# Kernel tuning notes

Measured on AMD Instinct MI355X. Metric: run time of the kernel, lower is better.

## Reference

```python
import jax, jax.numpy as jnp
import numpy as np

NUM_USER = 50000
NUM_ITEM = 40000
N = NUM_USER + NUM_ITEM
E_HALF = 500000
DIM = 64
NUM_ROUTING = 3
NEG_SLOPE = 0.01


def setup_inputs() -> dict:
    key = jax.random.key(0)
    ks = jax.random.split(key, 10)
    rng = np.random.default_rng(0)
    u = rng.integers(0, NUM_USER, E_HALF)
    it = rng.integers(NUM_USER, N, E_HALF)
    edge_index = jnp.asarray(
        np.stack([np.concatenate([u, it]), np.concatenate([it, u])]), dtype=jnp.int64
    )  # [2, 1M] bidirected user-item edges
    return {
        "edge_index": edge_index,
        "v_feat": jax.random.normal(ks[0], (NUM_ITEM, 2048), jnp.float32),
        "t_feat": jax.random.normal(ks[1], (NUM_ITEM, 384), jnp.float32),
        "pref_v": jax.random.normal(ks[2], (NUM_USER, DIM), jnp.float32),
        "pref_t": jax.random.normal(ks[3], (NUM_USER, DIM), jnp.float32),
        "W_v": jax.random.normal(ks[4], (2048, DIM), jnp.float32) * 0.02,
        "b_v": jnp.zeros((DIM,), jnp.float32),
        "W_t": jax.random.normal(ks[5], (384, DIM), jnp.float32) * 0.05,
        "b_t": jnp.zeros((DIM,), jnp.float32),
        "id_embedding": jax.random.normal(ks[6], (N, DIM), jnp.float32),
        "conf": jax.random.normal(ks[7], (N, 2), jnp.float32),
    }


def l2norm(x, eps=1e-12):
    n = jnp.sqrt(jnp.sum(x * x, axis=1, keepdims=True))
    return x / jnp.maximum(n, eps)


def leaky_relu(x):
    return jnp.where(x >= 0, x, NEG_SLOPE * x)


def segment_softmax(logits, seg, n):
    m = jax.ops.segment_max(logits, seg, num_segments=n)
    m = jnp.where(jnp.isfinite(m), m, 0.0)  # empty segments
    e = jnp.exp(logits - jax.lax.stop_gradient(m)[seg])
    s = jax.ops.segment_sum(e, seg, num_segments=n)
    return e / (s[seg] + 1e-16)


def gat_conv(x, ei):
    # dot-product attention, segment softmax over targets, scatter-add
    src, dst = ei[0], ei[1]
    xj = x[src]  # [E, D]
    alpha = jnp.sum(x[dst] * xj, axis=-1)  # [E]
    alpha = segment_softmax(alpha, dst, x.shape[0])
    out = jax.ops.segment_sum(xj * alpha[:, None], dst, num_segments=x.shape[0])
    return out, alpha


def sage_mean(x, ei, w):
    src, dst = ei[0], ei[1]
    msg = x[src] * w  # [E, D]
    s = jax.ops.segment_sum(msg, dst, num_segments=x.shape[0])
    cnt = jax.ops.segment_sum(jnp.ones((ei.shape[1],), x.dtype), dst, num_segments=x.shape[0])
    return s / jnp.maximum(cnt, 1.0)[:, None]


def cgcn(feat, pref, W, b, ei):
    features = l2norm(leaky_relu(feat @ W + b))  # [num_item, D]
    pref = l2norm(pref)
    for _ in range(NUM_ROUTING):
        x = jnp.concatenate([pref, features], axis=0)
        xh, _ = gat_conv(x, ei)
        pref = l2norm(pref + xh[:NUM_USER])
    x = jnp.concatenate([pref, features], axis=0)
    ei2 = jnp.concatenate([ei, ei[::-1]], axis=1)  # add reversed edges
    xh, alpha = gat_conv(x, ei2)
    return x + leaky_relu(xh), alpha[:, None]


def egcn(id_emb, ei, w):
    ei2 = jnp.concatenate([ei, ei[::-1]], axis=1)
    x = l2norm(id_emb)
    h1 = leaky_relu(sage_mean(x, ei2, w))
    h2 = leaky_relu(sage_mean(h1, ei2, w))
    return x + h1 + h2


def reference(edge_index, v_feat, t_feat, pref_v, pref_t, W_v, b_v, W_t, b_t,
              id_embedding, conf):
    v_rep, weight_v = cgcn(v_feat, pref_v, W_v, b_v, edge_index)
    t_rep, weight_t = cgcn(t_feat, pref_t, W_t, b_t, edge_index)
    content_rep = jnp.concatenate([v_rep, t_rep], axis=1)  # [N, 2D]
    weight = jnp.concatenate([weight_v, weight_t], axis=1)  # [2E, 2]
    # weight_mode == 'confid'
    confidence = jnp.concatenate([conf[edge_index[0]], conf[edge_index[1]]], axis=0)
    weight = jnp.max(weight * confidence, axis=1, keepdims=True)
    weight = jax.nn.relu(weight)  # pruning
    id_rep = egcn(id_embedding, edge_index, weight)
    return jnp.concatenate([id_rep, content_rep], axis=1)  # [N, 3D]
```

## Files before the change

kernel.cpp:

```cpp
#include <hip/hip_runtime.h>
#include <hip/hip_bf16.h>
#include <cstdint>
#include <cstddef>

#define NUSER 50000
#define NITEM 40000
#define NNODE 90000
#define NE    1000000
#define DIM   64
#define CAP   32

typedef __attribute__((ext_vector_type(8))) short short8;
typedef __attribute__((ext_vector_type(4))) float f32x4;

constexpr size_t O_XVT  = 0;
constexpr size_t O_X0   = 5760000;
constexpr size_t O_X0B  = 11520000;
constexpr size_t O_H1B  = 14400000;
constexpr size_t O_XVF  = 17280000;
constexpr size_t O_XTF  = 19840000;
constexpr size_t O_AE   = 22400000;
constexpr size_t O_BE   = 23400000;
constexpr size_t O_WE   = 24400000;
constexpr size_t O_SV   = 25400000;
constexpr size_t O_ST   = 25490000;
constexpr size_t O_DEG  = 25580000;
constexpr size_t O_RP   = 25670000;
constexpr size_t O_FILL = 25770000;
constexpr size_t O_SRC  = 25870000;
constexpr size_t O_BSUM = 26870000;
constexpr size_t O_BOFF = 26871000;
constexpr size_t O_WSPL = 26880000;
constexpr size_t SW_VHI = 0;
constexpr size_t SW_VLO = 131072;
constexpr size_t SW_THI = 262144;
constexpr size_t SW_TLO = 286720;

__device__ __forceinline__ float leaky(float x) { return x >= 0.f ? x : 0.01f * x; }

__device__ __forceinline__ unsigned short f2bfu(float x) {
  __hip_bfloat16 h = __float2bfloat16(x);
  return *reinterpret_cast<unsigned short*>(&h);
}
__device__ __forceinline__ short f2bf(float x) { return (short)f2bfu(x); }
__device__ __forceinline__ float bf2f(short s) {
  unsigned int u = ((unsigned int)(unsigned short)s) << 16;
  return __uint_as_float(u);
}
__device__ __forceinline__ void bf8_to_f32(uint4 u, float* f) {
  f[0] = __uint_as_float(u.x << 16); f[1] = __uint_as_float(u.x & 0xffff0000u);
  f[2] = __uint_as_float(u.y << 16); f[3] = __uint_as_float(u.y & 0xffff0000u);
// ... 7 lines not shown
  u.z = (uint32_t)f2bfu(f[4]) | ((uint32_t)f2bfu(f[5]) << 16);
  u.w = (uint32_t)f2bfu(f[6]) | ((uint32_t)f2bfu(f[7]) << 16);
  return u;
}
__device__ __forceinline__ void bf4_to_f32(uint2 u, float* f) {
  f[0] = __uint_as_float(u.x << 16); f[1] = __uint_as_float(u.x & 0xffff0000u);
  f[2] = __uint_as_float(u.y << 16); f[3] = __uint_as_float(u.y & 0xffff0000u);
}
__device__ __forceinline__ uint2 f32_to_bf4(const float* f) {
  uint2 u;
  u.x = (uint32_t)f2bfu(f[0]) | ((uint32_t)f2bfu(f[1]) << 16);
  u.y = (uint32_t)f2bfu(f[2]) | ((uint32_t)f2bfu(f[3]) << 16);
  return u;
}

__global__ void deg_count_kernel(const int* __restrict__ ei, int* __restrict__ deg) {
  int e = blockIdx.x * 256 + threadIdx.x;
  if (e >= NE) return;
  atomicAdd(&deg[ei[NE + e]], 1);
}

__global__ void block_sum_kernel(const int* __restrict__ deg, int* __restrict__ bsum) {
  __shared__ int sd[4];
  int i = blockIdx.x * 256 + threadIdx.x;
  int v = (i < NNODE) ? deg[i] : 0;
#pragma unroll
  for (int off = 32; off > 0; off >>= 1) v += __shfl_xor(v, off, 64);
  if ((threadIdx.x & 63) == 0) sd[threadIdx.x >> 6] = v;
  __syncthreads();
  if (threadIdx.x == 0) bsum[blockIdx.x] = sd[0] + sd[1] + sd[2] + sd[3];
}

__global__ void scan_bsum_kernel(const int* __restrict__ bsum, int* __restrict__ boff, int nb) {
  __shared__ int s[512];
  int t = threadIdx.x;
  int v = (t < nb) ? bsum[t] : 0;
  s[t] = v;
  __syncthreads();
  for (int off = 1; off < 512; off <<= 1) {
    int x = (t >= off) ? s[t - off] : 0;
    __syncthreads();
    s[t] += x;
    __syncthreads();
  }
  if (t < nb) boff[t] = s[t] - v;
}

__global__ void scan_final_kernel(const int* __restrict__ deg, const int* __restrict__ boff,
                                  int* __restrict__ row_ptr, int* __restrict__ fill) {
  __shared__ int s[256];
  int t = threadIdx.x;
  int i = blockIdx.x * 256 + t;
  int v = (i < NNODE) ? deg[i] : 0;
  s[t] = v;
  __syncthreads();
  for (int off = 1; off < 256; off <<= 1) {
    int x = (t >= off) ? s[t - off] : 0;
    __syncthreads();
    s[t] += x;
    __syncthreads();
  }
  int incl = s[t];
  int base = boff[blockIdx.x];
  if (i < NNODE) {
    row_ptr[i] = base + incl - v;
    fill[i] = base + incl - v;
    if (i == NNODE - 1) row_ptr[NNODE] = base + incl;
  }
}

__global__ void csr_fill_kernel(const int* __restrict__ ei, int* __restrict__ fill,
                                int* __restrict__ srcs) {
  int e = blockIdx.x * 256 + threadIdx.x;
  if (e >= NE) return;
  int s = ei[e], d = ei[NE + e];
  int slot = atomicAdd(&fill[d], 1);
  srcs[slot] = s;
}

__global__ void wsplit_kernel(const float* __restrict__ W, short* __restrict__ hi,
                              short* __restrict__ lo, int nelem) {
  int t = blockIdx.x * 256 + threadIdx.x;
  if (t >= nelem) return;
  int j = t & 7, sl = (t >> 3) & 15, q = (t >> 7) & 3, nt = (t >> 9) & 3, kt = t >> 11;
  int k = kt * 32 + q * 8 + j, n = nt * 16 + sl;
  float x = W[k * 64 + n];
  short h = f2bf(x);
  hi[t] = h;
  lo[t] = f2bf(x - bf2f(h));
}

__global__ __launch_bounds__(256) void gemm_mfma_kernel(const float* __restrict__ A,
                                                        const short* __restrict__ Whi,
                                                        const short* __restrict__ Wlo,
                                                        const float* __restrict__ bias,
                                                        float* __restrict__ outF,
                                                        unsigned short* __restrict__ xvt,
                                                        int colbase, int K) {
  __shared__ short Bsh[8192];
  __shared__ short Bsl[8192];
  int tid = threadIdx.x;
  int w = tid >> 6, lane = tid & 63, q = lane >> 4, sl = lane & 15;
  int m0 = blockIdx.x * 64;
  const float* arow = A + (size_t)(m0 + w * 16 + sl) * K;
  f32x4 acc[4] = {{0.f, 0.f, 0.f, 0.f}, {0.f, 0.f, 0.f, 0.f},
                  {0.f, 0.f, 0.f, 0.f}, {0.f, 0.f, 0.f, 0.f}};
  int nchunk = K >> 7;
  for (int c = 0; c < nchunk; ++c) {
    __syncthreads();
    const float4* srch = (const float4*)(Whi + (size_t)c * 8192);
    const float4* srcl = (const float4*)(Wlo + (size_t)c * 8192);
    float4* dsth = (float4*)Bsh;
    float4* dstl = (float4*)Bsl;
#pragma unroll
    for (int r = 0; r < 4; ++r) {
      dsth[r * 256 + tid] = srch[r * 256 + tid];
      dstl[r * 256 + tid] = srcl[r * 256 + tid];
    }
    __syncthreads();
#pragma unroll
    for (int kt = 0; kt < 4; ++kt) {
      int k = c * 128 + kt * 32 + q * 8;
// ... 5 lines not shown
      for (int j = 0; j < 8; ++j) {
        short h = f2bf(av[j]);
        ah[j] = h;
        al[j] = f2bf(av[j] - bf2f(h));
      }
#pragma unroll
      for (int nt = 0; nt < 4; ++nt) {
        short8 bh = *(short8*)&Bsh[(kt * 4 + nt) * 512 + lane * 8];
        short8 bl = *(short8*)&Bsl[(kt * 4 + nt) * 512 + lane * 8];
        acc[nt] = __builtin_amdgcn_mfma_f32_16x16x32_bf16(ah, bh, acc[nt], 0, 0, 0);
        acc[nt] = __builtin_amdgcn_mfma_f32_16x16x32_bf16(ah, bl, acc[nt], 0, 0, 0);
        acc[nt] = __builtin_amdgcn_mfma_f32_16x16x32_bf16(al, bh, acc[nt], 0, 0, 0);
      }
    }
  }
  float bnt[4];
#pragma unroll
  for (int nt = 0; nt < 4; ++nt) bnt[nt] = bias[nt * 16 + sl];
  float v[4][4];
#pragma unroll
  for (int nt = 0; nt < 4; ++nt)
#pragma unroll
    for (int i = 0; i < 4; ++i) v[nt][i] = leaky(acc[nt][i] + bnt[nt]);
#pragma unroll
  for (int i = 0; i < 4; ++i) {
    float ss = v[0][i] * v[0][i] + v[1][i] * v[1][i] + v[2][i] * v[2][i] + v[3][i] * v[3][i];
    ss += __shfl_xor(ss, 1);
    ss += __shfl_xor(ss, 2);
    ss += __shfl_xor(ss, 4);
    ss += __shfl_xor(ss, 8);
    float rinv = 1.f / fmaxf(sqrtf(ss), 1e-12f);
    int row = m0 + w * 16 + q * 4 + i;
#pragma unroll
    for (int nt = 0; nt < 4; ++nt) {
      float val = v[nt][i] * rinv;
      outF[(size_t)row * 64 + nt * 16 + sl] = val;
      xvt[(size_t)(NUSER + row) * 128 + colbase + nt * 16 + sl] = f2bfu(val);
    }
  }
}

__global__ __launch_bounds__(256) void l2norm_id_kernel(const float* __restrict__ id,
                                                        float* __restrict__ x0,
                                                        unsigned short* __restrict__ X0b) {
  int wid = (blockIdx.x * 256 + threadIdx.x) >> 6;
  int lane = threadIdx.x & 63, sub = lane >> 4, sl = lane & 15;
  int r = wid * 4 + sub;
  if (r >= NNODE) return;
  float4 v = *(const float4*)&id[(size_t)r * 64 + sl * 4];
  float ss = v.x * v.x + v.y * v.y + v.z * v.z + v.w * v.w;
  ss += __shfl_xor(ss, 1);
  ss += __shfl_xor(ss, 2);
  ss += __shfl_xor(ss, 4);
  ss += __shfl_xor(ss, 8);
  float rinv = 1.f / fmaxf(sqrtf(ss), 1e-12f);
  float f[4] = {v.x * rinv, v.y * rinv, v.z * rinv, v.w * rinv};
  *(float4*)&x0[(size_t)r * 64 + sl * 4] = *(float4*)f;
  *(uint2*)&X0b[(size_t)r * 64 + sl * 4] = f32_to_bf4(f);
}

__global__ __launch_bounds__(256) void routing_user_kernel(
    const float* __restrict__ pref_v, const float* __restrict__ pref_t,
    unsigned short* __restrict__ XVT,
    const int* __restrict__ rp, const int* __restrict__ srcs,
    const float* __restrict__ conf,
    float* __restrict__ Ae, float* __restrict__ Be,
    float* __restrict__ SV, float* __restrict__ ST,
    float* __restrict__ out) {
  __shared__ unsigned short cache[4][CAP * 128];
  int wv = threadIdx.x >> 6;
  int u = blockIdx.x * 4 + wv;
  if (u >= NUSER) return;
  int lane = threadIdx.x & 63;
  int sub = lane >> 4, sl = lane & 15, half = sl >> 3, e8 = sl & 7;
  unsigned short* myc = cache[wv];

  const float* psrc = half ? pref_t : pref_v;
  float p[8];
  *(float4*)&p[0] = *(const float4*)&psrc[(size_t)u * 64 + e8 * 8];
  *(float4*)&p[4] = *(const float4*)&psrc[(size_t)u * 64 + e8 * 8 + 4];
  float ss = 0.f;
#pragma unroll
  for (int k = 0; k < 8; ++k) ss += p[k] * p[k];
  ss += __shfl_xor(ss, 1); ss += __shfl_xor(ss, 2); ss += __shfl_xor(ss, 4);
  float rinv = 1.f / fmaxf(sqrtf(ss), 1e-12f);
#pragma unroll
  for (int k = 0; k < 8; ++k) p[k] *= rinv;

  int jb = rp[u], je = rp[u + 1], deg = je - jb;

  for (int it = 0; it < 3; ++it) {
    float S = 0.f;
    float acc[8] = {0.f, 0.f, 0.f, 0.f, 0.f, 0.f, 0.f, 0.f};
    for (int i0 = 0; i0 < deg; i0 += 4) {
      int i = i0 + sub;
      bool valid = i < deg;
      int ii = valid ? i : 0;
      int j = jb + ii;
      int s = srcs[j];
      uint4 u4;
      if (it == 0) {
        u4 = *(const uint4*)&XVT[(size_t)s * 128 + sl * 8];
        if (valid && i < CAP) *(uint4*)&myc[i * 128 + sl * 8] = u4;
      } else {
        if (ii < CAP) u4 = *(const uint4*)&myc[ii * 128 + sl * 8];
        else u4 = *(const uint4*)&XVT[(size_t)s * 128 + sl * 8];
      }
      float f[8];
      bf8_to_f32(u4, f);
      float d = 0.f;
#pragma unroll
      for (int k = 0; k < 8; ++k) d += p[k] * f[k];
      d += __shfl_xor(d, 1); d += __shfl_xor(d, 2); d += __shfl_xor(d, 4);
      float e = valid ? __expf(d) : 0.f;
      S += e;
#pragma unroll
      for (int k = 0; k < 8; ++k) acc[k] += e * f[k];
    }
    S += __shfl_xor(S, 16); S += __shfl_xor(S, 32);
#pragma unroll
    for (int k = 0; k < 8; ++k) {
      acc[k] += __shfl_xor(acc[k], 16);
      acc[k] += __shfl_xor(acc[k], 32);
    }
    if (deg > 0) {
      float r = 1.f / S;
#pragma unroll
      for (int k = 0; k < 8; ++k) p[k] += acc[k] * r;
    }
    ss = 0.f;
#pragma unroll
    for (int k = 0; k < 8; ++k) ss += p[k] * p[k];
    ss += __shfl_xor(ss, 1); ss += __shfl_xor(ss, 2); ss += __shfl_xor(ss, 4);
    rinv = 1.f / fmaxf(sqrtf(ss), 1e-12f);
#pragma unroll
    for (int k = 0; k < 8; ++k) p[k] *= rinv;
  }

  float S = 0.f;
  float acc[8] = {0.f, 0.f, 0.f, 0.f, 0.f, 0.f, 0.f, 0.f};
  for (int i0 = 0; i0 < deg; i0 += 4) {
    int i = i0 + sub;
    bool valid = i < deg;
    int ii = valid ? i : 0;
    int j = jb + ii;
    int s = srcs[j];
    uint4 u4;
    if (ii < CAP) u4 = *(const uint4*)&myc[ii * 128 + sl * 8];
    else u4 = *(const uint4*)&XVT[(size_t)s * 128 + sl * 8];
    float f[8];
    bf8_to_f32(u4, f);
    float d = 0.f;
#pragma unroll
    for (int k = 0; k < 8; ++k) d += p[k] * f[k];
    d += __shfl_xor(d, 1); d += __shfl_xor(d, 2); d += __shfl_xor(d, 4);
    float dot_o = __shfl_xor(d, 8);
    float e = valid ? __expf(d) : 0.f;
    S += e;
#pragma unroll
    for (int k = 0; k < 8; ++k) acc[k] += e * f[k];
    if (valid && sl == 0) {
      float2 c = *(const float2*)&conf[2 * s];
      Ae[j] = e * c.x;
      Be[j] = __expf(dot_o) * c.y;
    }
  }
  S += __shfl_xor(S, 16); S += __shfl_xor(S, 32);
#pragma unroll
  for (int k = 0; k < 8; ++k) {
    acc[k] += __shfl_xor(acc[k], 16);
    acc[k] += __shfl_xor(acc[k], 32);
  }
  float St = __shfl(S, 8);
  if (lane == 0) { SV[u] = S; ST[u] = St; }
  if (sub == 0) {
    float o[8];
    if (deg > 0) {
      float r = 1.f / S;
#pragma unroll
      for (int k = 0; k < 8; ++k) o[k] = p[k] + leaky(acc[k] * r);
    } else {
#pragma unroll
      for (int k = 0; k < 8; ++k) o[k] = p[k];
    }
    size_t ob = (size_t)u * 192 + 64 + half * 64 + e8 * 8;
    *(float4*)&out[ob] = *(float4*)&o[0];
    *(float4*)&out[ob + 4] = *(float4*)&o[4];
    *(uint4*)&XVT[(size_t)u * 128 + sl * 8] = f32_to_bf8(p);
  }
}

__global__ __launch_bounds__(256) void gat_item_kernel(
    const unsigned short* __restrict__ XVT,
    const float* __restrict__ XVf, const float* __restrict__ XTf,
    const int* __restrict__ rp, const int* __restrict__ srcs,
    const float* __restrict__ conf,
    float* __restrict__ Ae, float* __restrict__ Be,
    float* __restrict__ SV, float* __restrict__ ST,
    float* __restrict__ out) {
  int wid = (blockIdx.x * 256 + threadIdx.x) >> 6;
  if (wid >= NITEM) return;
  int lane = threadIdx.x & 63;
  int sub = lane >> 4, sl = lane & 15, half = sl >> 3, e8 = sl & 7;
  int row = NUSER + wid;
  const float* xsrc = half ? XTf : XVf;
  float xn[8];
  *(float4*)&xn[0] = *(const float4*)&xsrc[(size_t)wid * 64 + e8 * 8];
  *(float4*)&xn[4] = *(const float4*)&xsrc[(size_t)wid * 64 + e8 * 8 + 4];
  int jb = rp[row], je = rp[row + 1], deg = je - jb;
  float S = 0.f;
  float acc[8] = {0.f, 0.f, 0.f, 0.f, 0.f, 0.f, 0.f, 0.f};
  for (int i0 = 0; i0 < deg; i0 += 4) {
    int i = i0 + sub;
    bool valid = i < deg;
    int j = jb + (valid ? i : 0);
    int s = srcs[j];
    uint4 u4 = *(const uint4*)&XVT[(size_t)s * 128 + sl * 8];
    float f[8];
    bf8_to_f32(u4, f);
    float d = 0.f;
#pragma unroll
    for (int k = 0; k < 8; ++k) d += xn[k] * f[k];
    d += __shfl_xor(d, 1); d += __shfl_xor(d, 2); d += __shfl_xor(d, 4);
    float dot_o = __shfl_xor(d, 8);
    float e = valid ? __expf(d) : 0.f;
    S += e;
#pragma unroll
    for (int k = 0; k < 8; ++k) acc[k] += e * f[k];
    if (valid && sl == 0) {
      float2 c = *(const float2*)&conf[2 * s];
      Ae[j] = e * c.x;
      Be[j] = __expf(dot_o) * c.y;
    }
  }
  S += __shfl_xor(S, 16); S += __shfl_xor(S, 32);
#pragma unroll
  for (int k = 0; k < 8; ++k) {
    acc[k] += __shfl_xor(acc[k], 16);
    acc[k] += __shfl_xor(acc[k], 32);
  }
  float St = __shfl(S, 8);
  if (lane == 0) { SV[row] = S; ST[row] = St; }
  if (sub == 0) {
    float o[8];
    if (deg > 0) {
      float r = 1.f / S;
#pragma unroll
      for (int k = 0; k < 8; ++k) o[k] = xn[k] + leaky(acc[k] * r);
    } else {
#pragma unroll
      for (int k = 0; k < 8; ++k) o[k] = xn[k];
    }
    size_t ob = (size_t)row * 192 + 64 + half * 64 + e8 * 8;
    *(float4*)&out[ob] = *(float4*)&o[0];
    *(float4*)&out[ob + 4] = *(float4*)&o[4];
  }
}

__global__ __launch_bounds__(256) void egcn_h1_kernel(
    const unsigned short* __restrict__ X0b,
    const int* __restrict__ rp, const int* __restrict__ srcs,
    const float* __restrict__ Ae, const float* __restrict__ Be,
    const float* __restrict__ SV, const float* __restrict__ ST,
    float* __restrict__ wE, unsigned short* __restrict__ H1b) {
  int wid = (blockIdx.x * 256 + threadIdx.x) >> 6;
  if (wid >= NNODE) return;
  int lane = threadIdx.x & 63, sub = lane >> 4, sl = lane & 15;
  int jb = rp[wid], je = rp[wid + 1], deg = je - jb;
  float rv = 0.f, rt = 0.f;
  if (deg > 0) { rv = 0.5f / SV[wid]; rt = 0.5f / ST[wid]; }
  float acc[4] = {0.f, 0.f, 0.f, 0.f};
  for (int i0 = 0; i0 < deg; i0 += 4) {
    int i = i0 + sub;
    bool valid = i < deg;
    int j = jb + (valid ? i : 0);
    int s = srcs[j];
    float w = fmaxf(fmaxf(rv * Ae[j], rt * Be[j]), 0.f);
    if (!valid) w = 0.f;
    if (valid && sl == 0) wE[j] = w;
    uint2 u2 = *(const uint2*)&X0b[(size_t)s * 64 + sl * 4];
    float f[4];
    bf4_to_f32(u2, f);
#pragma unroll
    for (int k = 0; k < 4; ++k) acc[k] += w * f[k];
  }
#pragma unroll
  for (int k = 0; k < 4; ++k) {
    acc[k] += __shfl_xor(acc[k], 16);
    acc[k] += __shfl_xor(acc[k], 32);
  }
  if (sub == 0) {
    float h[4] = {0.f, 0.f, 0.f, 0.f};
    if (deg > 0) {
      float r = 1.f / (float)deg;
#pragma unroll
      for (int k = 0; k < 4; ++k) h[k] = leaky(acc[k] * r);
    }
    *(uint2*)&H1b[(size_t)wid * 64 + sl * 4] = f32_to_bf4(h);
  }
}

__global__ __launch_bounds__(256) void egcn_h2_kernel(
    const float* __restrict__ x0, const unsigned short* __restrict__ H1b,
    const int* __restrict__ rp, const int* __restrict__ srcs,
    const float* __restrict__ wE, float* __restrict__ out) {
  int wid = (blockIdx.x * 256 + threadIdx.x) >> 6;
  if (wid >= NNODE) return;
  int lane = threadIdx.x & 63, sub = lane >> 4, sl = lane & 15;
  int jb = rp[wid], je = rp[wid + 1], deg = je - jb;
  float acc[4] = {0.f, 0.f, 0.f, 0.f};
  for (int i0 = 0; i0 < deg; i0 += 4) {
    int i = i0 + sub;
    bool valid = i < deg;
    int j = jb + (valid ? i : 0);
    int s = srcs[j];
    float w = valid ? wE[j] : 0.f;
    uint2 u2 = *(const uint2*)&H1b[(size_t)s * 64 + sl * 4];
    float f[4];
    bf4_to_f32(u2, f);
#pragma unroll
    for (int k = 0; k < 4; ++k) acc[k] += w * f[k];
  }
#pragma unroll
  for (int k = 0; k < 4; ++k) {
    acc[k] += __shfl_xor(acc[k], 16);
    acc[k] += __shfl_xor(acc[k], 32);
  }
  if (sub == 0) {
    float h2[4] = {0.f, 0.f, 0.f, 0.f};
    if (deg > 0) {
      float r = 1.f / (float)deg;
#pragma unroll
      for (int k = 0; k < 4; ++k) h2[k] = leaky(acc[k] * r);
    }
    float4 a = *(const float4*)&x0[(size_t)wid * 64 + sl * 4];
    uint2 u2 = *(const uint2*)&H1b[(size_t)wid * 64 + sl * 4];
// ... 26 lines not shown
  float* x0 = ws + O_X0;
  unsigned short* X0b = (unsigned short*)(ws + O_X0B);
  unsigned short* H1b = (unsigned short*)(ws + O_H1B);
  float* XVf = ws + O_XVF;
  float* XTf = ws + O_XTF;
  float* Ae = ws + O_AE;
  float* Be = ws + O_BE;
  float* wE = ws + O_WE;
  float* SV = ws + O_SV;
  float* ST = ws + O_ST;
  int* deg = (int*)(ws + O_DEG);
  int* row_ptr = (int*)(ws + O_RP);
  int* fill = (int*)(ws + O_FILL);
  int* srcs = (int*)(ws + O_SRC);
  int* bsum = (int*)(ws + O_BSUM);
  int* boff = (int*)(ws + O_BOFF);
  short* wsp = (short*)(ws + O_WSPL);
  short* WvHi = wsp + SW_VHI;
  short* WvLo = wsp + SW_VLO;
  short* WtHi = wsp + SW_THI;
  short* WtLo = wsp + SW_TLO;

  const int NB = (NNODE + 255) / 256;

  hipMemsetAsync(deg, 0, NNODE * sizeof(int), stream);
  deg_count_kernel<<<(NE + 255) / 256, 256, 0, stream>>>(ei, deg);
  block_sum_kernel<<<NB, 256, 0, stream>>>(deg, bsum);
  scan_bsum_kernel<<<1, 512, 0, stream>>>(bsum, boff, NB);
  scan_final_kernel<<<NB, 256, 0, stream>>>(deg, boff, row_ptr, fill);
  csr_fill_kernel<<<(NE + 255) / 256, 256, 0, stream>>>(ei, fill, srcs);

  wsplit_kernel<<<(2048 * 64 + 255) / 256, 256, 0, stream>>>(W_v, WvHi, WvLo, 2048 * 64);
  wsplit_kernel<<<(384 * 64 + 255) / 256, 256, 0, stream>>>(W_t, WtHi, WtLo, 384 * 64);

  gemm_mfma_kernel<<<NITEM / 64, 256, 0, stream>>>(v_feat, WvHi, WvLo, b_v, XVf, XVT, 0, 2048);
  gemm_mfma_kernel<<<NITEM / 64, 256, 0, stream>>>(t_feat, WtHi, WtLo, b_t, XTf, XVT, 64, 384);

  l2norm_id_kernel<<<NNODE / 16, 256, 0, stream>>>(id_emb, x0, X0b);

  routing_user_kernel<<<NUSER / 4, 256, 0, stream>>>(pref_v, pref_t, XVT, row_ptr, srcs, conf,
                                                     Ae, Be, SV, ST, out);

  gat_item_kernel<<<NITEM / 4, 256, 0, stream>>>(XVT, XVf, XTf, row_ptr, srcs, conf,
                                                 Ae, Be, SV, ST, out);

  egcn_h1_kernel<<<NNODE / 4, 256, 0, stream>>>(X0b, row_ptr, srcs, Ae, Be, SV, ST, wE, H1b);
  egcn_h2_kernel<<<NNODE / 4, 256, 0, stream>>>(x0, H1b, row_ptr, srcs, wE, out);
}
```

Measured before the change: 973.0 us.

## Fuse preprocessing into mega kernel, split-K GEMM, fold EGCN h1 into GAT kernels

Several changes land together. Degree counting, l2norm of the id embeddings and both feature GEMMs now run as branches of one multi-role kernel, and the v_feat GEMM is split along K into four partial sums. The bias, leaky ReLU and l2norm epilogue moves into a separate kernel that also fills the CSR, and the scan is cut to two kernels. The EGCN h1 aggregation is folded into the user and item attention kernels, reading edge weights from a per-wave shared-memory stash, and the gather loops are unrolled by two. This removes launches and the separate h1 pass and spreads the GEMM over more blocks, at the cost of an extra partial-sum buffer round trip through memory.

Result: faster. 893.6 us (-8.2%).

```diff
diff --git a/kernel.cpp b/kernel.cpp
--- a/kernel.cpp
+++ b/kernel.cpp
@@ -9,6 +9,7 @@
 #define NE    1000000
 #define DIM   64
 #define CAP   32
+#define ESTN  128
 
 typedef __attribute__((ext_vector_type(8))) short short8;
 typedef __attribute__((ext_vector_type(4))) float f32x4;
@@ -29,12 +30,22 @@
 constexpr size_t O_FILL = 25770000;
 constexpr size_t O_SRC  = 25870000;
 constexpr size_t O_BSUM = 26870000;
-constexpr size_t O_BOFF = 26871000;
 constexpr size_t O_WSPL = 26880000;
+constexpr size_t O_PV   = 27040000;
+constexpr size_t O_PT   = 37280000;
 constexpr size_t SW_VHI = 0;
 constexpr size_t SW_VLO = 131072;
 constexpr size_t SW_THI = 262144;
 constexpr size_t SW_TLO = 286720;
+
+#define B_GV 2500
+#define B_GT 625
+#define B_DC 1024
+#define B_LN 1024
+#define BASE_GT 2500
+#define BASE_DC 3125
+#define BASE_LN 4149
+#define MEGA_BLOCKS 5173
 
 __device__ __forceinline__ float leaky(float x) { return x >= 0.f ? x : 0.01f * x; }
 
@@ -72,98 +83,36 @@
   return u;
 }
 
-__global__ void deg_count_kernel(const int* __restrict__ ei, int* __restrict__ deg) {
-  int e = blockIdx.x * 256 + threadIdx.x;
-  if (e >= NE) return;
-  atomicAdd(&deg[ei[NE + e]], 1);
-}
-
-__global__ void block_sum_kernel(const int* __restrict__ deg, int* __restrict__ bsum) {
-  __shared__ int sd[4];
-  int i = blockIdx.x * 256 + threadIdx.x;
-  int v = (i < NNODE) ? deg[i] : 0;
-#pragma unroll
-  for (int off = 32; off > 0; off >>= 1) v += __shfl_xor(v, off, 64);
-  if ((threadIdx.x & 63) == 0) sd[threadIdx.x >> 6] = v;
-  __syncthreads();
-  if (threadIdx.x == 0) bsum[blockIdx.x] = sd[0] + sd[1] + sd[2] + sd[3];
-}
-
-__global__ void scan_bsum_kernel(const int* __restrict__ bsum, int* __restrict__ boff, int nb) {
-  __shared__ int s[512];
-  int t = threadIdx.x;
-  int v = (t < nb) ? bsum[t] : 0;
-  s[t] = v;
-  __syncthreads();
-  for (int off = 1; off < 512; off <<= 1) {
-    int x = (t >= off) ? s[t - off] : 0;
-    __syncthreads();
-    s[t] += x;
-    __syncthreads();
-  }
-  if (t < nb) boff[t] = s[t] - v;
-}
-
-__global__ void scan_final_kernel(const int* __restrict__ deg, const int* __restrict__ boff,
-                                  int* __restrict__ row_ptr, int* __restrict__ fill) {
-  __shared__ int s[256];
-  int t = threadIdx.x;
-  int i = blockIdx.x * 256 + t;
-  int v = (i < NNODE) ? deg[i] : 0;
-  s[t] = v;
-  __syncthreads();
-  for (int off = 1; off < 256; off <<= 1) {
-    int x = (t >= off) ? s[t - off] : 0;
-    __syncthreads();
-    s[t] += x;
-    __syncthreads();
-  }
-  int incl = s[t];
-  int base = boff[blockIdx.x];
-  if (i < NNODE) {
-    row_ptr[i] = base + incl - v;
-    fill[i] = base + incl - v;
-    if (i == NNODE - 1) row_ptr[NNODE] = base + incl;
-  }
-}
-
-__global__ void csr_fill_kernel(const int* __restrict__ ei, int* __restrict__ fill,
-                                int* __restrict__ srcs) {
-  int e = blockIdx.x * 256 + threadIdx.x;
-  if (e >= NE) return;
-  int s = ei[e], d = ei[NE + e];
-  int slot = atomicAdd(&fill[d], 1);
-  srcs[slot] = s;
-}
-
-__global__ void wsplit_kernel(const float* __restrict__ W, short* __restrict__ hi,
-                              short* __restrict__ lo, int nelem) {
+__global__ __launch_bounds__(256) void wsplit_all_kernel(const float* __restrict__ Wv,
+                                                         const float* __restrict__ Wt,
+                                                         short* __restrict__ base) {
   int t = blockIdx.x * 256 + threadIdx.x;
-  if (t >= nelem) return;
-  int j = t & 7, sl = (t >> 3) & 15, q = (t >> 7) & 3, nt = (t >> 9) & 3, kt = t >> 11;
+  const int NV = 2048 * 64, NT = 384 * 64;
+  const float* W;
+  short *hi, *lo;
+  int idx;
+  if (t < NV) { W = Wv; hi = base + SW_VHI; lo = base + SW_VLO; idx = t; }
+  else if (t < NV + NT) { W = Wt; hi = base + SW_THI; lo = base + SW_TLO; idx = t - NV; }
+  else return;
+  int j = idx & 7, sl = (idx >> 3) & 15, q = (idx >> 7) & 3, nt = (idx >> 9) & 3, kt = idx >> 11;
   int k = kt * 32 + q * 8 + j, n = nt * 16 + sl;
   float x = W[k * 64 + n];
   short h = f2bf(x);
-  hi[t] = h;
-  lo[t] = f2bf(x - bf2f(h));
-}
-
-__global__ __launch_bounds__(256) void gemm_mfma_kernel(const float* __restrict__ A,
-                                                        const short* __restrict__ Whi,
-                                                        const short* __restrict__ Wlo,
-                                                        const float* __restrict__ bias,
-                                                        float* __restrict__ outF,
-                                                        unsigned short* __restrict__ xvt,
-                                                        int colbase, int K) {
-  __shared__ short Bsh[8192];
-  __shared__ short Bsl[8192];
+  hi[idx] = h;
+  lo[idx] = f2bf(x - bf2f(h));
+}
+
+__device__ __forceinline__ void gemm_partial(const float* __restrict__ A,
+                                             const short* __restrict__ Whi,
+                                             const short* __restrict__ Wlo,
+                                             float* __restrict__ P, size_t prow0,
+                                             short* Bsh, short* Bsl,
+                                             int m0, int K, int kofs, int nchunk) {
   int tid = threadIdx.x;
   int w = tid >> 6, lane = tid & 63, q = lane >> 4, sl = lane & 15;
-  int m0 = blockIdx.x * 64;
-  const float* arow = A + (size_t)(m0 + w * 16 + sl) * K;
+  const float* arow = A + (size_t)(m0 + w * 16 + sl) * K + kofs;
   f32x4 acc[4] = {{0.f, 0.f, 0.f, 0.f}, {0.f, 0.f, 0.f, 0.f},
                   {0.f, 0.f, 0.f, 0.f}, {0.f, 0.f, 0.f, 0.f}};
-  int nchunk = K >> 7;
   for (int c = 0; c < nchunk; ++c) {
     __syncthreads();
     const float4* srch = (const float4*)(Whi + (size_t)c * 8192);
@@ -199,66 +148,158 @@
       }
     }
   }
-  float bnt[4];
-#pragma unroll
-  for (int nt = 0; nt < 4; ++nt) bnt[nt] = bias[nt * 16 + sl];
-  float v[4][4];
-#pragma unroll
-  for (int nt = 0; nt < 4; ++nt)
-#pragma unroll
-    for (int i = 0; i < 4; ++i) v[nt][i] = leaky(acc[nt][i] + bnt[nt]);
 #pragma unroll
   for (int i = 0; i < 4; ++i) {
-    float ss = v[0][i] * v[0][i] + v[1][i] * v[1][i] + v[2][i] * v[2][i] + v[3][i] * v[3][i];
-    ss += __shfl_xor(ss, 1);
-    ss += __shfl_xor(ss, 2);
-    ss += __shfl_xor(ss, 4);
-    ss += __shfl_xor(ss, 8);
-    float rinv = 1.f / fmaxf(sqrtf(ss), 1e-12f);
     int row = m0 + w * 16 + q * 4 + i;
 #pragma unroll
-    for (int nt = 0; nt < 4; ++nt) {
-      float val = v[nt][i] * rinv;
-      outF[(size_t)row * 64 + nt * 16 + sl] = val;
-      xvt[(size_t)(NUSER + row) * 128 + colbase + nt * 16 + sl] = f2bfu(val);
-    }
-  }
-}
-
-__global__ __launch_bounds__(256) void l2norm_id_kernel(const float* __restrict__ id,
-                                                        float* __restrict__ x0,
-                                                        unsigned short* __restrict__ X0b) {
-  int wid = (blockIdx.x * 256 + threadIdx.x) >> 6;
-  int lane = threadIdx.x & 63, sub = lane >> 4, sl = lane & 15;
-  int r = wid * 4 + sub;
-  if (r >= NNODE) return;
-  float4 v = *(const float4*)&id[(size_t)r * 64 + sl * 4];
-  float ss = v.x * v.x + v.y * v.y + v.z * v.z + v.w * v.w;
-  ss += __shfl_xor(ss, 1);
-  ss += __shfl_xor(ss, 2);
-  ss += __shfl_xor(ss, 4);
-  ss += __shfl_xor(ss, 8);
+    for (int nt = 0; nt < 4; ++nt)
+      P[(prow0 + row) * 64 + nt * 16 + sl] = acc[nt][i];
+  }
+}
+
+__global__ __launch_bounds__(256) void mega_prep_kernel(
+    const float* __restrict__ v_feat, const float* __restrict__ t_feat,
+    const short* __restrict__ wsp,
+    const int* __restrict__ ei, int* __restrict__ deg,
+    const float* __restrict__ id_emb, float* __restrict__ x0,
+    unsigned short* __restrict__ X0b,
+    float* __restrict__ Pv, float* __restrict__ Pt) {
+  __shared__ short Bsh[8192];
+  __shared__ short Bsl[8192];
+  int b = blockIdx.x;
+  if (b < B_GV) {
+    int seg = b / 625, m0 = (b % 625) * 64;
+    gemm_partial(v_feat, wsp + SW_VHI + (size_t)seg * 4 * 8192,
+                 wsp + SW_VLO + (size_t)seg * 4 * 8192,
+                 Pv, (size_t)seg * 40000, Bsh, Bsl, m0, 2048, seg * 512, 4);
+  } else if (b < BASE_DC) {
+    int m0 = (b - BASE_GT) * 64;
+    gemm_partial(t_feat, wsp + SW_THI, wsp + SW_TLO, Pt, 0, Bsh, Bsl, m0, 384, 0, 3);
+  } else if (b < BASE_LN) {
+    for (int e = (b - BASE_DC) * 256 + threadIdx.x; e < NE; e += B_DC * 256)
+      atomicAdd(&deg[ei[NE + e]], 1);
+  } else {
+    int sl = threadIdx.x & 15;
+    int qg = (b - BASE_LN) * 16 + (threadIdx.x >> 4);
+    for (int r = qg; r < NNODE; r += B_LN * 16) {
+      float4 v = *(const float4*)&id_emb[(size_t)r * 64 + sl * 4];
+      float ss = v.x * v.x + v.y * v.y + v.z * v.z + v.w * v.w;
+      ss += __shfl_xor(ss, 1); ss += __shfl_xor(ss, 2);
+      ss += __shfl_xor(ss, 4); ss += __shfl_xor(ss, 8);
+      float rinv = 1.f / fmaxf(sqrtf(ss), 1e-12f);
+      float f[4] = {v.x * rinv, v.y * rinv, v.z * rinv, v.w * rinv};
+      *(float4*)&x0[(size_t)r * 64 + sl * 4] = *(float4*)f;
+      *(uint2*)&X0b[(size_t)r * 64 + sl * 4] = f32_to_bf4(f);
+    }
+  }
+}
+
+__global__ __launch_bounds__(256) void scan_a_kernel(const int* __restrict__ deg,
+                                                     int* __restrict__ bsum) {
+  __shared__ int sd[4];
+  int i = blockIdx.x * 256 + threadIdx.x;
+  int v = (i < NNODE) ? deg[i] : 0;
+#pragma unroll
+  for (int off = 32; off > 0; off >>= 1) v += __shfl_xor(v, off, 64);
+  if ((threadIdx.x & 63) == 0) sd[threadIdx.x >> 6] = v;
+  __syncthreads();
+  if (threadIdx.x == 0) bsum[blockIdx.x] = sd[0] + sd[1] + sd[2] + sd[3];
+}
+
+__global__ __launch_bounds__(256) void scan_b_kernel(const int* __restrict__ deg,
+                                                     const int* __restrict__ bsum,
+                                                     int* __restrict__ row_ptr,
+                                                     int* __restrict__ fill) {
+  __shared__ int s[256];
+  __shared__ int sbase[4];
+  int t = threadIdx.x, b = blockIdx.x;
+  int v = (t < b) ? bsum[t] : 0;
+  if (t + 256 < b) v += bsum[t + 256];
+#pragma unroll
+  for (int off = 32; off > 0; off >>= 1) v += __shfl_xor(v, off, 64);
+  if ((t & 63) == 0) sbase[t >> 6] = v;
+  int i = b * 256 + t;
+  int d = (i < NNODE) ? deg[i] : 0;
+  s[t] = d;
+  __syncthreads();
+  int base = sbase[0] + sbase[1] + sbase[2] + sbase[3];
+  for (int off = 1; off < 256; off <<= 1) {
+    int x = (t >= off) ? s[t - off] : 0;
+    __syncthreads();
+    s[t] += x;
+    __syncthreads();
+  }
+  if (i < NNODE) {
+    int excl = base + s[t] - d;
+    row_ptr[i] = excl;
+    fill[i] = excl;
+    if (i == NNODE - 1) row_ptr[NNODE] = base + s[t];
+  }
+}
+
+#define FE_FILL 512
+__global__ __launch_bounds__(256) void fill_epi_kernel(
+    const int* __restrict__ ei, int* __restrict__ fill, int* __restrict__ srcs,
+    const float* __restrict__ Pv, const float* __restrict__ Pt,
+    const float* __restrict__ b_v, const float* __restrict__ b_t,
+    float* __restrict__ XVf, float* __restrict__ XTf,
+    unsigned short* __restrict__ XVT) {
+  int b = blockIdx.x;
+  if (b < FE_FILL) {
+    for (int e = b * 256 + threadIdx.x; e < NE; e += FE_FILL * 256) {
+      int s = ei[e], d = ei[NE + e];
+      int slot = atomicAdd(&fill[d], 1);
+      srcs[slot] = s;
+    }
+    return;
+  }
+  int sl = threadIdx.x & 15;
+  int q = (b - FE_FILL) * 16 + (threadIdx.x >> 4);
+  if (q >= 80000) return;
+  int mod = q >= 40000;
+  int r = q - mod * 40000;
+  float4 a;
+  if (!mod) {
+    a = *(const float4*)&Pv[(size_t)r * 64 + sl * 4];
+#pragma unroll
+    for (int seg = 1; seg < 4; ++seg) {
+      float4 p = *(const float4*)&Pv[((size_t)seg * 40000 + r) * 64 + sl * 4];
+      a.x += p.x; a.y += p.y; a.z += p.z; a.w += p.w;
+    }
+  } else {
+    a = *(const float4*)&Pt[(size_t)r * 64 + sl * 4];
+  }
+  float4 bias = *(const float4*)&(mod ? b_t : b_v)[sl * 4];
+  float f[4] = {leaky(a.x + bias.x), leaky(a.y + bias.y),
+                leaky(a.z + bias.z), leaky(a.w + bias.w)};
+  float ss = f[0] * f[0] + f[1] * f[1] + f[2] * f[2] + f[3] * f[3];
+  ss += __shfl_xor(ss, 1); ss += __shfl_xor(ss, 2);
+  ss += __shfl_xor(ss, 4); ss += __shfl_xor(ss, 8);
   float rinv = 1.f / fmaxf(sqrtf(ss), 1e-12f);
-  float f[4] = {v.x * rinv, v.y * rinv, v.z * rinv, v.w * rinv};
-  *(float4*)&x0[(size_t)r * 64 + sl * 4] = *(float4*)f;
-  *(uint2*)&X0b[(size_t)r * 64 + sl * 4] = f32_to_bf4(f);
+#pragma unroll
+  for (int k = 0; k < 4; ++k) f[k] *= rinv;
+  *(float4*)&(mod ? XTf : XVf)[(size_t)r * 64 + sl * 4] = *(float4*)f;
+  *(uint2*)&XVT[(size_t)(NUSER + r) * 128 + mod * 64 + sl * 4] = f32_to_bf4(f);
 }
 
 __global__ __launch_bounds__(256) void routing_user_kernel(
     const float* __restrict__ pref_v, const float* __restrict__ pref_t,
-    unsigned short* __restrict__ XVT,
+    unsigned short* __restrict__ XVT, const unsigned short* __restrict__ X0b,
     const int* __restrict__ rp, const int* __restrict__ srcs,
     const float* __restrict__ conf,
     float* __restrict__ Ae, float* __restrict__ Be,
     float* __restrict__ SV, float* __restrict__ ST,
+    float* __restrict__ wE, unsigned short* __restrict__ H1b,
     float* __restrict__ out) {
   __shared__ unsigned short cache[4][CAP * 128];
+  __shared__ float estash[4][2 * ESTN];
   int wv = threadIdx.x >> 6;
   int u = blockIdx.x * 4 + wv;
   if (u >= NUSER) return;
   int lane = threadIdx.x & 63;
   int sub = lane >> 4, sl = lane & 15, half = sl >> 3, e8 = sl & 7;
   unsigned short* myc = cache[wv];
+  float* es = estash[wv];
 
   const float* psrc = half ? pref_t : pref_v;
   float p[8];
@@ -277,30 +318,37 @@
   for (int it = 0; it < 3; ++it) {
     float S = 0.f;
     float acc[8] = {0.f, 0.f, 0.f, 0.f, 0.f, 0.f, 0.f, 0.f};
-    for (int i0 = 0; i0 < deg; i0 += 4) {
-      int i = i0 + sub;
-      bool valid = i < deg;
-      int ii = valid ? i : 0;
-      int j = jb + ii;
-      int s = srcs[j];
-      uint4 u4;
+    for (int i0 = 0; i0 < deg; i0 += 8) {
+      int iA = i0 + sub, iB = i0 + 4 + sub;
+      bool vA = iA < deg, vB = iB < deg;
+      int jA = jb + (vA ? iA : 0), jB = jb + (vB ? iB : 0);
+      uint4 uA, uB;
       if (it == 0) {
-        u4 = *(const uint4*)&XVT[(size_t)s * 128 + sl * 8];
-        if (valid && i < CAP) *(uint4*)&myc[i * 128 + sl * 8] = u4;
+        int sA = srcs[jA], sB = srcs[jB];
+        uA = *(const uint4*)&XVT[(size_t)sA * 128 + sl * 8];
+        uB = *(const uint4*)&XVT[(size_t)sB * 128 + sl * 8];
+        if (vA && iA < CAP) *(uint4*)&myc[iA * 128 + sl * 8] = uA;
+        if (vB && iB < CAP) *(uint4*)&myc[iB * 128 + sl * 8] = uB;
       } else {
-        if (ii < CAP) u4 = *(const uint4*)&myc[ii * 128 + sl * 8];
-        else u4 = *(const uint4*)&XVT[(size_t)s * 128 + sl * 8];
+        int iiA = vA ? iA : 0, iiB = vB ? iB : 0;
+        if (iiA < CAP) uA = *(const uint4*)&myc[iiA * 128 + sl * 8];
+        else uA = *(const uint4*)&XVT[(size_t)srcs[jA] * 128 + sl * 8];
+        if (iiB < CAP) uB = *(const uint4*)&myc[iiB * 128 + sl * 8];
+        else uB = *(const uint4*)&XVT[(size_t)srcs[jB] * 128 + sl * 8];
       }
-      float f[8];
-      bf8_to_f32(u4, f);
-      float d = 0.f;
-#pragma unroll
-      for (int k = 0; k < 8; ++k) d += p[k] * f[k];
-      d += __shfl_xor(d, 1); d += __shfl_xor(d, 2); d += __shfl_xor(d, 4);
-      float e = valid ? __expf(d) : 0.f;
-      S += e;
-#pragma unroll
-      for (int k = 0; k < 8; ++k) acc[k] += e * f[k];
+      float fA[8], fB[8];
+      bf8_to_f32(uA, fA);
+      bf8_to_f32(uB, fB);
+      float dA = 0.f, dB = 0.f;
+#pragma unroll
+      for (int k = 0; k < 8; ++k) { dA += p[k] * fA[k]; dB += p[k] * fB[k]; }
+      dA += __shfl_xor(dA, 1); dA += __shfl_xor(dA, 2); dA += __shfl_xor(dA, 4);
+      dB += __shfl_xor(dB, 1); dB += __shfl_xor(dB, 2); dB += __shfl_xor(dB, 4);
+      float eA = vA ? __expf(dA) : 0.f;
+      float eB = vB ? __expf(dB) : 0.f;
+      S += eA + eB;
+#pragma unroll
+      for (int k = 0; k < 8; ++k) acc[k] += eA * fA[k] + eB * fB[k];
     }
     S += __shfl_xor(S, 16); S += __shfl_xor(S, 32);
 #pragma unroll
@@ -324,30 +372,44 @@
 
   float S = 0.f;
   float acc[8] = {0.f, 0.f, 0.f, 0.f, 0.f, 0.f, 0.f, 0.f};
-  for (int i0 = 0; i0 < deg; i0 += 4) {
-    int i = i0 + sub;
-    bool valid = i < deg;
-    int ii = valid ? i : 0;
-    int j = jb + ii;
-    int s = srcs[j];
-    uint4 u4;
-    if (ii < CAP) u4 = *(const uint4*)&myc[ii * 128 + sl * 8];
-    else u4 = *(const uint4*)&XVT[(size_t)s * 128 + sl * 8];
-    float f[8];
-    bf8_to_f32(u4, f);
-    float d = 0.f;
-#pragma unroll
-    for (int k = 0; k < 8; ++k) d += p[k] * f[k];
-    d += __shfl_xor(d, 1); d += __shfl_xor(d, 2); d += __shfl_xor(d, 4);
-    float dot_o = __shfl_xor(d, 8);
-    float e = valid ? __expf(d) : 0.f;
-    S += e;
-#pragma unroll
-    for (int k = 0; k < 8; ++k) acc[k] += e * f[k];
-    if (valid && sl == 0) {
-      float2 c = *(const float2*)&conf[2 * s];
-      Ae[j] = e * c.x;
-      Be[j] = __expf(dot_o) * c.y;
+  for (int i0 = 0; i0 < deg; i0 += 8) {
+    int iA = i0 + sub, iB = i0 + 4 + sub;
+    bool vA = iA < deg, vB = iB < deg;
+    int jA = jb + (vA ? iA : 0), jB = jb + (vB ? iB : 0);
+    int sA = srcs[jA], sB = srcs[jB];
+    int iiA = vA ? iA : 0, iiB = vB ? iB : 0;
+    uint4 uA, uB;
+    if (iiA < CAP) uA = *(const uint4*)&myc[iiA * 128 + sl * 8];
+    else uA = *(const uint4*)&XVT[(size_t)sA * 128 + sl * 8];
+    if (iiB < CAP) uB = *(const uint4*)&myc[iiB * 128 + sl * 8];
+    else uB = *(const uint4*)&XVT[(size_t)sB * 128 + sl * 8];
+    float fA[8], fB[8];
+    bf8_to_f32(uA, fA);
+    bf8_to_f32(uB, fB);
+    float dA = 0.f, dB = 0.f;
+#pragma unroll
+    for (int k = 0; k < 8; ++k) { dA += p[k] * fA[k]; dB += p[k] * fB[k]; }
+    dA += __shfl_xor(dA, 1); dA += __shfl_xor(dA, 2); dA += __shfl_xor(dA, 4);
+    dB += __shfl_xor(dB, 1); dB += __shfl_xor(dB, 2); dB += __shfl_xor(dB, 4);
+    float dAo = __shfl_xor(dA, 8), dBo = __shfl_xor(dB, 8);
+    float eA = vA ? __expf(dA) : 0.f;
+    float eB = vB ? __expf(dB) : 0.f;
+    S += eA + eB;
+#pragma unroll
+    for (int k = 0; k < 8; ++k) acc[k] += eA * fA[k] + eB * fB[k];
+    if (sl == 0) {
+      if (vA) {
+        float2 c = *(const float2*)&conf[2 * sA];
+        float ae = eA * c.x, be = __expf(dAo) * c.y;
+        Ae[jA] = ae; Be[jA] = be;
+        if (iA < ESTN) { es[2 * iA] = ae; es[2 * iA + 1] = be; }
+      }
+      if (vB) {
+        float2 c = *(const float2*)&conf[2 * sB];
+        float ae = eB * c.x, be = __expf(dBo) * c.y;
+        Ae[jB] = ae; Be[jB] = be;
+        if (iB < ESTN) { es[2 * iB] = ae; es[2 * iB + 1] = be; }
+      }
     }
   }
   S += __shfl_xor(S, 16); S += __shfl_xor(S, 32);
@@ -356,8 +418,8 @@
     acc[k] += __shfl_xor(acc[k], 16);
     acc[k] += __shfl_xor(acc[k], 32);
   }
-  float St = __shfl(S, 8);
-  if (lane == 0) { SV[u] = S; ST[u] = St; }
+  float So = __shfl_xor(S, 8);
+  if (lane == 0) { SV[u] = S; ST[u] = So; }
   if (sub == 0) {
     float o[8];
     if (deg > 0) {
@@ -373,20 +435,68 @@
     *(float4*)&out[ob + 4] = *(float4*)&o[4];
     *(uint4*)&XVT[(size_t)u * 128 + sl * 8] = f32_to_bf8(p);
   }
+
+  float Sv = half ? So : S;
+  float St_ = half ? S : So;
+  float rv = (deg > 0) ? 0.5f / Sv : 0.f;
+  float rt = (deg > 0) ? 0.5f / St_ : 0.f;
+  float hacc[4] = {0.f, 0.f, 0.f, 0.f};
+  for (int i0 = 0; i0 < deg; i0 += 8) {
+    int iA = i0 + sub, iB = i0 + 4 + sub;
+    bool vA = iA < deg, vB = iB < deg;
+    int jA = jb + (vA ? iA : 0), jB = jb + (vB ? iB : 0);
+    int sA = srcs[jA], sB = srcs[jB];
+    uint2 gA = *(const uint2*)&X0b[(size_t)sA * 64 + sl * 4];
+    uint2 gB = *(const uint2*)&X0b[(size_t)sB * 64 + sl * 4];
+    int iiA = vA ? iA : 0, iiB = vB ? iB : 0;
+    float aeA = (iiA < ESTN) ? es[2 * iiA] : Ae[jA];
+    float beA = (iiA < ESTN) ? es[2 * iiA + 1] : Be[jA];
+    float aeB = (iiB < ESTN) ? es[2 * iiB] : Ae[jB];
+    float beB = (iiB < ESTN) ? es[2 * iiB + 1] : Be[jB];
+    float wA = vA ? fmaxf(fmaxf(rv * aeA, rt * beA), 0.f) : 0.f;
+    float wB = vB ? fmaxf(fmaxf(rv * aeB, rt * beB), 0.f) : 0.f;
+    if (sl == 0) {
+      if (vA) wE[jA] = wA;
+      if (vB) wE[jB] = wB;
+    }
+    float fA[4], fB[4];
+    bf4_to_f32(gA, fA);
+    bf4_to_f32(gB, fB);
+#pragma unroll
+    for (int k = 0; k < 4; ++k) hacc[k] += wA * fA[k] + wB * fB[k];
+  }
+#pragma unroll
+  for (int k = 0; k < 4; ++k) {
+    hacc[k] += __shfl_xor(hacc[k], 16);
+    hacc[k] += __shfl_xor(hacc[k], 32);
+  }
+  if (sub == 0) {
+    float h[4] = {0.f, 0.f, 0.f, 0.f};
+    if (deg > 0) {
+      float r = 1.f / (float)deg;
+#pragma unroll
+      for (int k = 0; k < 4; ++k) h[k] = leaky(hacc[k] * r);
+    }
+    *(uint2*)&H1b[(size_t)u * 64 + sl * 4] = f32_to_bf4(h);
+  }
 }
 
 __global__ __launch_bounds__(256) void gat_item_kernel(
-    const unsigned short* __restrict__ XVT,
+    const unsigned short* __restrict__ XVT, const unsigned short* __restrict__ X0b,
     const float* __restrict__ XVf, const float* __restrict__ XTf,
     const int* __restrict__ rp, const int* __restrict__ srcs,
     const float* __restrict__ conf,
     float* __restrict__ Ae, float* __restrict__ Be,
     float* __restrict__ SV, float* __restrict__ ST,
+    float* __restrict__ wE, unsigned short* __restrict__ H1b,
     float* __restrict__ out) {
-  int wid = (blockIdx.x * 256 + threadIdx.x) >> 6;
+  __shared__ float estash[4][2 * ESTN];
+  int wv = threadIdx.x >> 6;
+  int wid = blockIdx.x * 4 + wv;
   if (wid >= NITEM) return;
   int lane = threadIdx.x & 63;
   int sub = lane >> 4, sl = lane & 15, half = sl >> 3, e8 = sl & 7;
+  float* es = estash[wv];
   int row = NUSER + wid;
   const float* xsrc = half ? XTf : XVf;
   float xn[8];
@@ -395,27 +505,40 @@
   int jb = rp[row], je = rp[row + 1], deg = je - jb;
   float S = 0.f;
   float acc[8] = {0.f, 0.f, 0.f, 0.f, 0.f, 0.f, 0.f, 0.f};
-  for (int i0 = 0; i0 < deg; i0 += 4) {
-    int i = i0 + sub;
-    bool valid = i < deg;
-    int j = jb + (valid ? i : 0);
-    int s = srcs[j];
-    uint4 u4 = *(const uint4*)&XVT[(size_t)s * 128 + sl * 8];
-    float f[8];
-    bf8_to_f32(u4, f);
-    float d = 0.f;
-#pragma unroll
-    for (int k = 0; k < 8; ++k) d += xn[k] * f[k];
-    d += __shfl_xor(d, 1); d += __shfl_xor(d, 2); d += __shfl_xor(d, 4);
-    float dot_o = __shfl_xor(d, 8);
-    float e = valid ? __expf(d) : 0.f;
-    S += e;
-#pragma unroll
-    for (int k = 0; k < 8; ++k) acc[k] += e * f[k];
-    if (valid && sl == 0) {
-      float2 c = *(const float2*)&conf[2 * s];
-      Ae[j] = e * c.x;
-      Be[j] = __expf(dot_o) * c.y;
+  for (int i0 = 0; i0 < deg; i0 += 8) {
+    int iA = i0 + sub, iB = i0 + 4 + sub;
+    bool vA = iA < deg, vB = iB < deg;
+    int jA = jb + (vA ? iA : 0), jB = jb + (vB ? iB : 0);
+    int sA = srcs[jA], sB = srcs[jB];
+    uint4 uA = *(const uint4*)&XVT[(size_t)sA * 128 + sl * 8];
+    uint4 uB = *(const uint4*)&XVT[(size_t)sB * 128 + sl * 8];
+    float fA[8], fB[8];
+    bf8_to_f32(uA, fA);
+    bf8_to_f32(uB, fB);
+    float dA = 0.f, dB = 0.f;
+#pragma unroll
+    for (int k = 0; k < 8; ++k) { dA += xn[k] * fA[k]; dB += xn[k] * fB[k]; }
+    dA += __shfl_xor(dA, 1); dA += __shfl_xor(dA, 2); dA += __shfl_xor(dA, 4);
+    dB += __shfl_xor(dB, 1); dB += __shfl_xor(dB, 2); dB += __shfl_xor(dB, 4);
+    float dAo = __shfl_xor(dA, 8), dBo = __shfl_xor(dB, 8);
+    float eA = vA ? __expf(dA) : 0.f;
+    float eB = vB ? __expf(dB) : 0.f;
+    S += eA + eB;
+#pragma unroll
+    for (int k = 0; k < 8; ++k) acc[k] += eA * fA[k] + eB * fB[k];
+    if (sl == 0) {
+      if (vA) {
+        float2 c = *(const float2*)&conf[2 * sA];
+        float ae = eA * c.x, be = __expf(dAo) * c.y;
+        Ae[jA] = ae; Be[jA] = be;
+        if (iA < ESTN) { es[2 * iA] = ae; es[2 * iA + 1] = be; }
+      }
+      if (vB) {
+        float2 c = *(const float2*)&conf[2 * sB];
+        float ae = eB * c.x, be = __expf(dBo) * c.y;
+        Ae[jB] = ae; Be[jB] = be;
+        if (iB < ESTN) { es[2 * iB] = ae; es[2 * iB + 1] = be; }
+      }
     }
   }
   S += __shfl_xor(S, 16); S += __shfl_xor(S, 32);
@@ -424,8 +547,8 @@
     acc[k] += __shfl_xor(acc[k], 16);
     acc[k] += __shfl_xor(acc[k], 32);
   }
-  float St = __shfl(S, 8);
-  if (lane == 0) { SV[row] = S; ST[row] = St; }
+  float So = __shfl_xor(S, 8);
+  if (lane == 0) { SV[row] = S; ST[row] = So; }
   if (sub == 0) {
     float o[8];
     if (deg > 0) {
@@ -440,48 +563,49 @@
     *(float4*)&out[ob] = *(float4*)&o[0];
     *(float4*)&out[ob + 4] = *(float4*)&o[4];
   }
-}
-
-__global__ __launch_bounds__(256) void egcn_h1_kernel(
-    const unsigned short* __restrict__ X0b,
-    const int* __restrict__ rp, const int* __restrict__ srcs,
-    const float* __restrict__ Ae, const float* __restrict__ Be,
-    const float* __restrict__ SV, const float* __restrict__ ST,
-    float* __restrict__ wE, unsigned short* __restrict__ H1b) {
-  int wid = (blockIdx.x * 256 + threadIdx.x) >> 6;
-  if (wid >= NNODE) return;
-  int lane = threadIdx.x & 63, sub = lane >> 4, sl = lane & 15;
-  int jb = rp[wid], je = rp[wid + 1], deg = je - jb;
-  float rv = 0.f, rt = 0.f;
-  if (deg > 0) { rv = 0.5f / SV[wid]; rt = 0.5f / ST[wid]; }
-  float acc[4] = {0.f, 0.f, 0.f, 0.f};
-  for (int i0 = 0; i0 < deg; i0 += 4) {
-    int i = i0 + sub;
-    bool valid = i < deg;
-    int j = jb + (valid ? i : 0);
-    int s = srcs[j];
-    float w = fmaxf(fmaxf(rv * Ae[j], rt * Be[j]), 0.f);
-    if (!valid) w = 0.f;
-    if (valid && sl == 0) wE[j] = w;
-    uint2 u2 = *(const uint2*)&X0b[(size_t)s * 64 + sl * 4];
-    float f[4];
-    bf4_to_f32(u2, f);
-#pragma unroll
-    for (int k = 0; k < 4; ++k) acc[k] += w * f[k];
+
+  float Sv = half ? So : S;
+  float St_ = half ? S : So;
+  float rv = (deg > 0) ? 0.5f / Sv : 0.f;
+  float rt = (deg > 0) ? 0.5f / St_ : 0.f;
+  float hacc[4] = {0.f, 0.f, 0.f, 0.f};
+  for (int i0 = 0; i0 < deg; i0 += 8) {
+    int iA = i0 + sub, iB = i0 + 4 + sub;
+    bool vA = iA < deg, vB = iB < deg;
+    int jA = jb + (vA ? iA : 0), jB = jb + (vB ? iB : 0);
+    int sA = srcs[jA], sB = srcs[jB];
+    uint2 gA = *(const uint2*)&X0b[(size_t)sA * 64 + sl * 4];
+    uint2 gB = *(const uint2*)&X0b[(size_t)sB * 64 + sl * 4];
+    int iiA = vA ? iA : 0, iiB = vB ? iB : 0;
+    float aeA = (iiA < ESTN) ? es[2 * iiA] : Ae[jA];
+    float beA = (iiA < ESTN) ? es[2 * iiA + 1] : Be[jA];
+    float aeB = (iiB < ESTN) ? es[2 * iiB] : Ae[jB];
+    float beB = (iiB < ESTN) ? es[2 * iiB + 1] : Be[jB];
+    float wA = vA ? fmaxf(fmaxf(rv * aeA, rt * beA), 0.f) : 0.f;
+    float wB = vB ? fmaxf(fmaxf(rv * aeB, rt * beB), 0.f) : 0.f;
+    if (sl == 0) {
+      if (vA) wE[jA] = wA;
+      if (vB) wE[jB] = wB;
+    }
+    float fA[4], fB[4];
+    bf4_to_f32(gA, fA);
+    bf4_to_f32(gB, fB);
+#pragma unroll
+    for (int k = 0; k < 4; ++k) hacc[k] += wA * fA[k] + wB * fB[k];
   }
 #pragma unroll
   for (int k = 0; k < 4; ++k) {
-    acc[k] += __shfl_xor(acc[k], 16);
-    acc[k] += __shfl_xor(acc[k], 32);
+    hacc[k] += __shfl_xor(hacc[k], 16);
+    hacc[k] += __shfl_xor(hacc[k], 32);
   }
   if (sub == 0) {
     float h[4] = {0.f, 0.f, 0.f, 0.f};
     if (deg > 0) {
       float r = 1.f / (float)deg;
 #pragma unroll
-      for (int k = 0; k < 4; ++k) h[k] = leaky(acc[k] * r);
-    }
-    *(uint2*)&H1b[(size_t)wid * 64 + sl * 4] = f32_to_bf4(h);
+      for (int k = 0; k < 4; ++k) h[k] = leaky(hacc[k] * r);
+    }
+    *(uint2*)&H1b[(size_t)row * 64 + sl * 4] = f32_to_bf4(h);
   }
 }
 
@@ -494,17 +618,20 @@
   int lane = threadIdx.x & 63, sub = lane >> 4, sl = lane & 15;
   int jb = rp[wid], je = rp[wid + 1], deg = je - jb;
   float acc[4] = {0.f, 0.f, 0.f, 0.f};
-  for (int i0 = 0; i0 < deg; i0 += 4) {
-    int i = i0 + sub;
-    bool valid = i < deg;
-    int j = jb + (valid ? i : 0);
-    int s = srcs[j];
-    float w = valid ? wE[j] : 0.f;
-    uint2 u2 = *(const uint2*)&H1b[(size_t)s * 64 + sl * 4];
-    float f[4];
-    bf4_to_f32(u2, f);
-#pragma unroll
-    for (int k = 0; k < 4; ++k) acc[k] += w * f[k];
+  for (int i0 = 0; i0 < deg; i0 += 8) {
+    int iA = i0 + sub, iB = i0 + 4 + sub;
+    bool vA = iA < deg, vB = iB < deg;
+    int jA = jb + (vA ? iA : 0), jB = jb + (vB ? iB : 0);
+    int sA = srcs[jA], sB = srcs[jB];
+    float wA = vA ? wE[jA] : 0.f;
+    float wB = vB ? wE[jB] : 0.f;
+    uint2 gA = *(const uint2*)&H1b[(size_t)sA * 64 + sl * 4];
+    uint2 gB = *(const uint2*)&H1b[(size_t)sB * 64 + sl * 4];
+    float fA[4], fB[4];
+    bf4_to_f32(gA, fA);
+    bf4_to_f32(gB, fB);
+#pragma unroll
+    for (int k = 0; k < 4; ++k) acc[k] += wA * fA[k] + wB * fB[k];
   }
 #pragma unroll
   for (int k = 0; k < 4; ++k) {
@@ -561,36 +688,23 @@
   int* fill = (int*)(ws + O_FILL);
   int* srcs = (int*)(ws + O_SRC);
   int* bsum = (int*)(ws + O_BSUM);
-  int* boff = (int*)(ws + O_BOFF);
   short* wsp = (short*)(ws + O_WSPL);
-  short* WvHi = wsp + SW_VHI;
-  short* WvLo = wsp + SW_VLO;
-  short* WtHi = wsp + SW_THI;
-  short* WtLo = wsp + SW_TLO;
+  float* Pv = ws + O_PV;
+  float* Pt = ws + O_PT;
 
   const int NB = (NNODE + 255) / 256;
 
   hipMemsetAsync(deg, 0, NNODE * sizeof(int), stream);
-  deg_count_kernel<<<(NE + 255) / 256, 256, 0, stream>>>(ei, deg);
-  block_sum_kernel<<<NB, 256, 0, stream>>>(deg, bsum);
-  scan_bsum_kernel<<<1, 512, 0, stream>>>(bsum, boff, NB);
-  scan_final_kernel<<<NB, 256, 0, stream>>>(deg, boff, row_ptr, fill);
-  csr_fill_kernel<<<(NE + 255) / 256, 256, 0, stream>>>(ei, fill, srcs);
-
-  wsplit_kernel<<<(2048 * 64 + 255) / 256, 256, 0, stream>>>(W_v, WvHi, WvLo, 2048 * 64);
-  wsplit_kernel<<<(384 * 64 + 255) / 256, 256, 0, stream>>>(W_t, WtHi, WtLo, 384 * 64);
-
-  gemm_mfma_kernel<<<NITEM / 64, 256, 0, stream>>>(v_feat, WvHi, WvLo, b_v, XVf, XVT, 0, 2048);
-  gemm_mfma_kernel<<<NITEM / 64, 256, 0, stream>>>(t_feat, WtHi, WtLo, b_t, XTf, XVT, 64, 384);
-
-  l2norm_id_kernel<<<NNODE / 16, 256, 0, stream>>>(id_emb, x0, X0b);
-
-  routing_user_kernel<<<NUSER / 4, 256, 0, stream>>>(pref_v, pref_t, XVT, row_ptr, srcs, conf,
-                                                     Ae, Be, SV, ST, out);
-
-  gat_item_kernel<<<NITEM / 4, 256, 0, stream>>>(XVT, XVf, XTf, row_ptr, srcs, conf,
-                                                 Ae, Be, SV, ST, out);
-
-  egcn_h1_kernel<<<NNODE / 4, 256, 0, stream>>>(X0b, row_ptr, srcs, Ae, Be, SV, ST, wE, H1b);
+  wsplit_all_kernel<<<(2048 * 64 + 384 * 64 + 255) / 256, 256, 0, stream>>>(W_v, W_t, wsp);
+  mega_prep_kernel<<<MEGA_BLOCKS, 256, 0, stream>>>(v_feat, t_feat, wsp, ei, deg,
+                                                    id_emb, x0, X0b, Pv, Pt);
+  scan_a_kernel<<<NB, 256, 0, stream>>>(deg, bsum);
+  scan_b_kernel<<<NB, 256, 0, stream>>>(deg, bsum, row_ptr, fill);
+  fill_epi_kernel<<<FE_FILL + 5000, 256, 0, stream>>>(ei, fill, srcs, Pv, Pt, b_v, b_t,
+                                                      XVf, XTf, XVT);
+  routing_user_kernel<<<NUSER / 4, 256, 0, stream>>>(pref_v, pref_t, XVT, X0b, row_ptr,
+                                                     srcs, conf, Ae, Be, SV, ST, wE, H1b, out);
+  gat_item_kernel<<<NITEM / 4, 256, 0, stream>>>(XVT, X0b, XVf, XTf, row_ptr, srcs, conf,
+                                                 Ae, Be, SV, ST, wE, H1b, out);
   egcn_h2_kernel<<<NNODE / 4, 256, 0, stream>>>(x0, H1b, row_ptr, srcs, wE, out);
 }
```
